# Kernel optimization log

Hardware: AMD Instinct MI355X
Metric: run time of the kernel (lower is better)

## Reference

```python
import jax, jax.numpy as jnp
import numpy as np

D_MODEL, D_STATE, D_CONV, EXPAND = 1024, 16, 4, 2
D_INNER = EXPAND * D_MODEL
B, L = 2, 2048


def setup_inputs() -> dict:
    key = jax.random.key(0)
    ks = jax.random.split(key, 8)
    s = lambda fan: 1.0 / np.sqrt(fan)
    x = jax.random.normal(ks[0], (B, L, D_MODEL), dtype=jnp.float32)
    W_in = jax.random.normal(ks[1], (2 * D_INNER, D_MODEL), dtype=jnp.float32) * s(D_MODEL)
    conv_w = jax.random.normal(ks[2], (D_INNER, 1, D_CONV), dtype=jnp.float32) * s(D_CONV)
    conv_b = jax.random.normal(ks[3], (D_INNER,), dtype=jnp.float32) * 0.01
    A_log = jnp.log(jnp.abs(jax.random.normal(ks[4], (D_INNER, D_STATE), dtype=jnp.float32)) + 1e-4)
    Dp = jnp.ones((D_INNER,), dtype=jnp.float32)
    W_dt = jax.random.normal(ks[5], (D_INNER, D_INNER), dtype=jnp.float32) * s(D_INNER)
    b_dt = jax.random.normal(ks[6], (D_INNER,), dtype=jnp.float32) * 0.01
    W_out = jax.random.normal(ks[7], (D_MODEL, D_INNER), dtype=jnp.float32) * s(D_INNER)
    return {"x": x, "W_in": W_in, "conv_w": conv_w, "conv_b": conv_b,
            "A_log": A_log, "Dp": Dp, "W_dt": W_dt, "b_dt": b_dt, "W_out": W_out}


def _mamba_fwd(x, W_in, conv_w, conv_b, A_log, Dp, W_dt, b_dt, W_out):
    Bsz, Ln, _ = x.shape
    xz = x @ W_in.T                                  # [B, L, 2*d_inner]
    x_proj, z = jnp.split(xz, 2, axis=-1)            # each [B, L, d_inner]
    # depthwise causal conv1d: left-pad d_conv-1 (matches torch pad + [:L] slice)
    xc = jnp.transpose(x_proj, (0, 2, 1))            # [B, C, L]
    xc = jax.lax.conv_general_dilated(
        xc, conv_w, window_strides=(1,), padding=[(D_CONV - 1, 0)],
        dimension_numbers=("NCH", "OIH", "NCH"), feature_group_count=D_INNER)
    xc = xc + conv_b[None, :, None]
    x_act = jax.nn.silu(jnp.transpose(xc, (0, 2, 1)))  # [B, L, d_inner]
    dt = jax.nn.softplus(x_act @ W_dt.T + b_dt)        # [B, L, d_inner]
    A = -jnp.exp(A_log)                                # [d_inner, d_state]

    def step(h, inp):
        xt, dt_t = inp                                 # [B, d_inner] each
        dA = jnp.exp(dt_t[:, :, None] * A[None])       # [B, d_inner, d_state]
        dB = (dt_t * xt)[:, :, None]                   # broadcast over states
        h = dA * h + dB
        y_t = h.sum(axis=-1) + Dp * xt                 # [B, d_inner]
        return h, y_t

    h0 = jnp.zeros((Bsz, D_INNER, D_STATE), dtype=x.dtype)
    xs = (jnp.transpose(x_act, (1, 0, 2)), jnp.transpose(dt, (1, 0, 2)))  # [L, B, d_inner]
    _, ys = jax.lax.scan(step, h0, xs)
    y_ssm = jnp.transpose(ys, (1, 0, 2))               # [B, L, d_inner]
    y_gated = y_ssm * jax.nn.silu(z)
    return y_gated @ W_out.T                           # [B, L, d_model]


def reference(x, W_in, conv_w, conv_b, A_log, Dp, W_dt, b_dt, W_out):
    return _mamba_fwd(x, W_in, conv_w, conv_b, A_log, Dp, W_dt, b_dt, W_out)
```

## Files before the change

### kernel.cpp

```cpp
#include <hip/hip_runtime.h>

#define DMODEL 1024
#define DSTATE 16
#define DCONV  4
#define DINNER 2048
#define BSZ    2
#define LSEQ   2048
#define MTOT   (BSZ * LSEQ)
#define NCH    64
#define LC     (LSEQ / NCH)
#define LOG2E  1.44269504088896f

typedef unsigned short u16;
typedef __attribute__((ext_vector_type(8))) short short8;
typedef __attribute__((ext_vector_type(8))) unsigned short u16x8;
typedef __attribute__((ext_vector_type(4))) float f32x4;

__device__ __forceinline__ float silu_f(float v) {
  return v * __builtin_amdgcn_rcpf(1.f + __builtin_amdgcn_exp2f(-v * LOG2E));
}

__device__ __forceinline__ u16 f2bf(float f) {
  unsigned int u = __float_as_uint(f);
  u += 0x7FFF + ((u >> 16) & 1);
  return (u16)(u >> 16);
}
__device__ __forceinline__ float bf2f(u16 b) { return __uint_as_float(((unsigned int)b) << 16); }

__device__ __forceinline__ void gload_lds16(const u16* g, u16* l) {
  __builtin_amdgcn_global_load_lds((const __attribute__((address_space(1))) unsigned int*)g,
                                   (__attribute__((address_space(3))) unsigned int*)l, 16, 0, 0);
}

__global__ __launch_bounds__(256)
void cast4(const float4* __restrict__ s0, ushort4* __restrict__ d0, int n0,
           const float4* __restrict__ s1, ushort4* __restrict__ d1, int n1,
           const float4* __restrict__ s2, ushort4* __restrict__ d2, int n2,
           const float4* __restrict__ s3, ushort4* __restrict__ d3, int n3) {
  int i = blockIdx.x * 256 + threadIdx.x;
  const float4* s; ushort4* d;
  if (i < n0)                { s = s0; d = d0; }
  else if ((i -= n0) < n1)   { s = s1; d = d1; }
  else if ((i -= n1) < n2)   { s = s2; d = d2; }
  else if ((i -= n2) < n3)   { s = s3; d = d3; }
  else return;
  float4 v = s[i];
  ushort4 o = { f2bf(v.x), f2bf(v.y), f2bf(v.z), f2bf(v.w) };
  d[i] = o;
}

template<int OBF>
__global__ __launch_bounds__(256, 2)
void hgemm256(const u16* __restrict__ A, const u16* __restrict__ B,
              void* __restrict__ Cv, int M, int N, int K) {
  __shared__ u16 As[256 * 64];
  __shared__ u16 Bs[128 * 64];
  const int tid  = threadIdx.x;
  const int lane = tid & 63;
  const int w    = tid >> 6;
  const int quad = lane >> 4;
  const int l16  = lane & 15;

  const int nbn = N >> 7, nbm = M >> 8;
  const int pid = blockIdx.x;
  const int npg = 4 * nbn;
  const int fm  = (pid / npg) * 4;
  const int gsz = (nbm - fm < 4) ? (nbm - fm) : 4;
  const int bm  = (fm + (pid % gsz)) << 8;
  const int bn  = ((pid % npg) / gsz) << 7;

  const int wm = (w & 1) * 128;
  const int wn = (w >> 1) * 64;

  const int rseg = lane >> 3;
  const int cd   = (lane & 7) ^ rseg;
  const u16* Gp[12]; u16* Lp[12];
#pragma unroll
  for (int q = 0; q < 12; ++q) {
    const int g = w * 12 + q;
    if (g < 32) {
      const int r = g * 8 + rseg;
      Gp[q] = A + (size_t)(bm + r) * K + (cd << 3);
      Lp[q] = &As[g << 9];
    } else {
      const int r = (g - 32) * 8 + rseg;
      Gp[q] = B + (size_t)(bn + r) * K + (cd << 3);
      Lp[q] = &Bs[(g - 32) << 9];
    }
  }

  const short8* Afp[8][2];
  const short8* Bfp[4][2];
#pragma unroll
  for (int t = 0; t < 8; ++t) {
    const int ra = wm + 16 * t + l16;
#pragma unroll
    for (int ks = 0; ks < 2; ++ks)
      Afp[t][ks] = (const short8*)&As[ra * 64 + (((quad + 4 * ks) ^ (ra & 7)) << 3)];
  }
#pragma unroll
  for (int t = 0; t < 4; ++t) {
    const int rb = wn + 16 * t + l16;
#pragma unroll
    for (int ks = 0; ks < 2; ++ks)
      Bfp[t][ks] = (const short8*)&Bs[rb * 64 + (((quad + 4 * ks) ^ (rb & 7)) << 3)];
  }

  f32x4 acc[8][4] = {};

  for (int k0 = 0; k0 < K; k0 += 64) {
#pragma unroll
    for (int q = 0; q < 12; ++q) { gload_lds16(Gp[q], Lp[q]); Gp[q] += 64; }
    __syncthreads();
#pragma unroll
    for (int ks = 0; ks < 2; ++ks) {
      short8 af[8], bf[4];
#pragma unroll
      for (int t = 0; t < 8; ++t) af[t] = *Afp[t][ks];
#pragma unroll
      for (int t = 0; t < 4; ++t) bf[t] = *Bfp[t][ks];
#pragma unroll
      for (int ti = 0; ti < 8; ++ti)
#pragma unroll
        for (int tj = 0; tj < 4; ++tj)
          acc[ti][tj] = __builtin_amdgcn_mfma_f32_16x16x32_bf16(af[ti], bf[tj],
                                                                acc[ti][tj], 0, 0, 0);
    }
    __syncthreads();
  }

#pragma unroll
  for (int ti = 0; ti < 8; ++ti) {
    const int row0 = bm + wm + 16 * ti + quad * 4;
#pragma unroll
    for (int tj = 0; tj < 4; ++tj) {
      const int col = bn + wn + 16 * tj + l16;
#pragma unroll
      for (int i = 0; i < 4; ++i) {
        const float v = acc[ti][tj][i];
        if (OBF) ((u16*)Cv)[(size_t)(row0 + i) * N + col] = f2bf(v);
        else     ((float*)Cv)[(size_t)(row0 + i) * N + col] = v;
      }
    }
  }
}

template<int MODE, int OBF, int BN>
__global__ __launch_bounds__(256)
void hgemm_bk128(const u16* __restrict__ A, const u16* __restrict__ B,
                 const float* __restrict__ bias, void* __restrict__ Cv,
                 int M, int N, int K) {
  constexpr int ASEG = 32;
  constexpr int BSEG = BN / 4;
  constexpr int SPW  = (ASEG + BSEG) / 4;
  constexpr int BT   = BN / 32;
  __shared__ u16 As[128 * 128];
  __shared__ u16 Bs[BN * 128];
  const int tid  = threadIdx.x;
  const int lane = tid & 63;
  const int w    = tid >> 6;
  const int quad = lane >> 4;
  const int l16  = lane & 15;

  const int nbn = N / BN, nbm = M >> 7;
  const int pid = blockIdx.x;
  const int npg = 4 * nbn;
  const int fm  = (pid / npg) * 4;
  const int gsz = (nbm - fm < 4) ? (nbm - fm) : 4;
  const int bm  = (fm + (pid % gsz)) << 7;
  const int bn  = ((pid % npg) / gsz) * BN;

  const int wm = (w & 1) * 64;
  const int wn = (w >> 1) * (BN / 2);

  const int rs4 = lane >> 4;
  const u16* Gp[SPW]; u16* Lp[SPW];
#pragma unroll
  for (int q = 0; q < SPW; ++q) {
    const int g = w * SPW + q;
    if (g < ASEG) {
      const int r  = g * 4 + rs4;
      const int cdk = (lane & 15) ^ (r & 15);
      Gp[q] = A + (size_t)(bm + r) * K + (cdk << 3);
      Lp[q] = &As[g << 9];
    } else {
      const int r  = (g - ASEG) * 4 + rs4;
      const int cdk = (lane & 15) ^ (r & 15);
      Gp[q] = B + (size_t)(bn + r) * K + (cdk << 3);
      Lp[q] = &Bs[(g - ASEG) << 9];
    }
  }

  const short8* Afp[4][4];
  const short8* Bfp[BT][4];
#pragma unroll
  for (int t = 0; t < 4; ++t) {
    const int ra = wm + 16 * t + l16;
#pragma unroll
    for (int ks = 0; ks < 4; ++ks)
      Afp[t][ks] = (const short8*)&As[ra * 128 + (((quad + 4 * ks) ^ (ra & 15)) << 3)];
  }
#pragma unroll
  for (int t = 0; t < BT; ++t) {
    const int rb = wn + 16 * t + l16;
#pragma unroll
    for (int ks = 0; ks < 4; ++ks)
      Bfp[t][ks] = (const short8*)&Bs[rb * 128 + (((quad + 4 * ks) ^ (rb & 15)) << 3)];
  }

  f32x4 acc[4][BT] = {};

  for (int k0 = 0; k0 < K; k0 += 128) {
#pragma unroll
    for (int q = 0; q < SPW; ++q) { gload_lds16(Gp[q], Lp[q]); Gp[q] += 128; }
    __syncthreads();
#pragma unroll
    for (int ks = 0; ks < 4; ++ks) {
      short8 af[4], bf[BT];
#pragma unroll
      for (int t = 0; t < 4; ++t) af[t] = *Afp[t][ks];
#pragma unroll
      for (int t = 0; t < BT; ++t) bf[t] = *Bfp[t][ks];
#pragma unroll
      for (int ti = 0; ti < 4; ++ti)
#pragma unroll
        for (int tj = 0; tj < BT; ++tj)
          acc[ti][tj] = __builtin_amdgcn_mfma_f32_16x16x32_bf16(af[ti], bf[tj],
                                                                acc[ti][tj], 0, 0, 0);
    }
    __syncthreads();
  }

#pragma unroll
  for (int ti = 0; ti < 4; ++ti) {
    const int row0 = bm + wm + 16 * ti + quad * 4;
#pragma unroll
    for (int tj = 0; tj < BT; ++tj) {
      const int col = bn + wn + 16 * tj + l16;
      const float bv = (MODE == 1) ? bias[col] : 0.f;
#pragma unroll
      for (int i = 0; i < 4; ++i) {
        float v = acc[ti][tj][i] + bv;
        if (MODE == 1) v = (v > 20.f) ? v : __logf(1.f + __expf(v));
        if (OBF) ((u16*)Cv)[(size_t)(row0 + i) * N + col] = f2bf(v);
        else     ((float*)Cv)[(size_t)(row0 + i) * N + col] = v;
      }
    }
  }
}

__global__ __launch_bounds__(256)
void conv_silu(const u16* __restrict__ xz, const float* __restrict__ conv_w,
               const float* __restrict__ conv_b, u16* __restrict__ xact) {
  const int i = blockIdx.x * 256 + threadIdx.x;
  const int ko = i & 255;
  const int t  = (i >> 8) & (LSEQ - 1);
  const int b  = i >> 19;
  const int c  = ko << 3;
  float a[8];
  float4 w[8];
#pragma unroll
  for (int j = 0; j < 8; ++j) {
    a[j] = conv_b[c + j];
    w[j] = *(const float4*)(conv_w + (c + j) * DCONV);
  }
#pragma unroll
  for (int k = 0; k < DCONV; ++k) {
    const int tt = t + k - (DCONV - 1);
    if (tt >= 0) {
      const u16x8 v = *(const u16x8*)(xz + ((size_t)(b * LSEQ + tt) << 12) + c);
#pragma unroll
      for (int j = 0; j < 8; ++j)
        a[j] = fmaf(bf2f(v[j]), ((const float*)&w[j])[k], a[j]);
    }
  }
  u16x8 o;
#pragma unroll
  for (int j = 0; j < 8; ++j) o[j] = f2bf(silu_f(a[j]));
  *(u16x8*)(xact + ((size_t)(b * LSEQ + t) << 11) + c) = o;
}


__global__ __launch_bounds__(256, 2)
void scan_pass1(const u16* __restrict__ dtb, const u16* __restrict__ xact,
                const float* __restrict__ A_log,
                u16* __restrict__ hbuf, float* __restrict__ sumdt) {
  const int gid = blockIdx.x * 256 + threadIdx.x;
  const int c  = gid & (DINNER - 1);
  const int ch = (gid >> 11) & (NCH - 1);
  const int b  = gid >> 17;
  float a2[16];
#pragma unroll
  for (int s = 0; s < 16; ++s)
    a2[s] = -__expf(A_log[c * DSTATE + s]) * LOG2E;
  const size_t base = ((size_t)(b * LSEQ + ch * LC) << 11) + c;
  float h[16] = {};
  float sd = 0.f;
  for (int j = 0; j < LC; j += 2) {
    const float dt0 = bf2f(dtb [base + ((size_t)j << 11)]);
    const float xv0 = bf2f(xact[base + ((size_t)j << 11)]);
    const float dt1 = bf2f(dtb [base + ((size_t)(j + 1) << 11)]);
    const float xv1 = bf2f(xact[base + ((size_t)(j + 1) << 11)]);
    const float dx0 = dt0 * xv0, dx1 = dt1 * xv1;
    sd += dt0 + dt1;
#pragma unroll
    for (int s = 0; s < 16; ++s)
      h[s] = fmaf(__builtin_amdgcn_exp2f(dt0 * a2[s]), h[s], dx0);
#pragma unroll
    for (int s = 0; s < 16; ++s)
      h[s] = fmaf(__builtin_amdgcn_exp2f(dt1 * a2[s]), h[s], dx1);
  }
  u16x8* ho = (u16x8*)&hbuf[(((size_t)(b * NCH + ch) * DINNER) + c) << 4];
  u16x8 lo, hi;
#pragma unroll
  for (int s = 0; s < 8; ++s) { lo[s] = f2bf(h[s]); hi[s] = f2bf(h[8 + s]); }
  ho[0] = lo; ho[1] = hi;
  sumdt[(size_t)(b * NCH + ch) * DINNER + c] = sd;
}

__global__ __launch_bounds__(256)
void scan_combine(u16* __restrict__ hbuf, const float* __restrict__ sumdt,
                  const float* __restrict__ A_log) {
  const int gid = blockIdx.x * 256 + threadIdx.x;
  const int s = gid & 15;
  const int c = (gid >> 4) & (DINNER - 1);
  const int b = gid >> 15;
  const float a2 = -__expf(A_log[c * DSTATE + s]) * LOG2E;
  float h = 0.f;
  for (int k = 0; k < NCH; ++k) {
    const size_t o = (((size_t)(b * NCH + k) * DINNER) + c) * 16 + s;
    const float he = bf2f(hbuf[o]);
    const float sd = sumdt[(size_t)(b * NCH + k) * DINNER + c];
    hbuf[o] = f2bf(h);
    h = fmaf(__builtin_amdgcn_exp2f(sd * a2), h, he);
  }
}

__global__ __launch_bounds__(256, 2)
void scan_pass3(const u16* __restrict__ dtb, const u16* __restrict__ xact,
                const u16* __restrict__ xz, const float* __restrict__ A_log,
                const float* __restrict__ Dp, const u16* __restrict__ hbuf,
                u16* __restrict__ yg) {
  const int gid = blockIdx.x * 256 + threadIdx.x;
  const int c  = gid & (DINNER - 1);
  const int ch = (gid >> 11) & (NCH - 1);
  const int b  = gid >> 17;
  float a2[16];
#pragma unroll
  for (int s = 0; s < 16; ++s)
    a2[s] = -__expf(A_log[c * DSTATE + s]) * LOG2E;
  const float dp = Dp[c];
  float h[16];
  const u16x8* hi = (const u16x8*)&hbuf[(((size_t)(b * NCH + ch) * DINNER) + c) << 4];
  const u16x8 vlo = hi[0], vhi = hi[1];
#pragma unroll
  for (int s = 0; s < 8; ++s) { h[s] = bf2f(vlo[s]); h[8 + s] = bf2f(vhi[s]); }
  const size_t base  = ((size_t)(b * LSEQ + ch * LC) << 11) + c;
  const size_t zbase = ((size_t)(b * LSEQ + ch * LC) << 12) + DINNER + c;
  for (int j = 0; j < LC; j += 2) {
    const float dt0 = bf2f(dtb [base + ((size_t)j << 11)]);
    const float xv0 = bf2f(xact[base + ((size_t)j << 11)]);
    const float zv0 = bf2f(xz[zbase + ((size_t)j << 12)]);
    const float dt1 = bf2f(dtb [base + ((size_t)(j + 1) << 11)]);
    const float xv1 = bf2f(xact[base + ((size_t)(j + 1) << 11)]);
    const float zv1 = bf2f(xz[zbase + ((size_t)(j + 1) << 12)]);
    const float dx0 = dt0 * xv0, dx1 = dt1 * xv1;
    float y0 = 0.f, y1 = 0.f;
#pragma unroll
    for (int s = 0; s < 16; ++s) {
      h[s] = fmaf(__builtin_amdgcn_exp2f(dt0 * a2[s]), h[s], dx0);
      y0 += h[s];
    }
#pragma unroll
    for (int s = 0; s < 16; ++s) {
      h[s] = fmaf(__builtin_amdgcn_exp2f(dt1 * a2[s]), h[s], dx1);
      y1 += h[s];
    }
    y0 = fmaf(dp, xv0, y0);
    y1 = fmaf(dp, xv1, y1);
    yg[base + ((size_t)j << 11)]       = f2bf(y0 * silu_f(zv0));
    yg[base + ((size_t)(j + 1) << 11)] = f2bf(y1 * silu_f(zv1));
  }
}

extern "C" void kernel_launch(void* const* d_in, const int* in_sizes, int n_in,
                              void* d_out, int out_size, void* d_ws, size_t ws_size,
                              hipStream_t stream) {
  const float* x      = (const float*)d_in[0];
  const float* W_in   = (const float*)d_in[1];
  const float* conv_w = (const float*)d_in[2];
  const float* conv_b = (const float*)d_in[3];
  const float* A_log  = (const float*)d_in[4];
  const float* Dp     = (const float*)d_in[5];
  const float* W_dt   = (const float*)d_in[6];
  const float* b_dt   = (const float*)d_in[7];
  const float* W_out  = (const float*)d_in[8];
  float* out = (float*)d_out;

  u16* xz   = (u16*)d_ws;
  u16* dtb  = xz   + (size_t)MTOT * 2 * DINNER;
  u16* xbf  = dtb  + (size_t)MTOT * DINNER;
  u16* wibf = xbf  + (size_t)MTOT * DMODEL;
  u16* wdbf = wibf + (size_t)2 * DINNER * DMODEL;
  u16* wobf = wdbf + (size_t)DINNER * DINNER;
  u16* xact = wobf + (size_t)DMODEL * DINNER;
  u16* yg   = xact + (size_t)MTOT * DINNER;
  u16* hbuf = yg   + (size_t)MTOT * DINNER;
  float* sumdt = (float*)(hbuf + (size_t)BSZ * NCH * DINNER * 16);

  const dim3 blk(256);

  const int n0 = MTOT * DMODEL / 4, n1 = 2 * DINNER * DMODEL / 4;
  const int n2 = DINNER * DINNER / 4, n3 = DMODEL * DINNER / 4;
  cast4<<<(n0 + n1 + n2 + n3) / 256, blk, 0, stream>>>(
      (const float4*)x, (ushort4*)xbf, n0,
      (const float4*)W_in, (ushort4*)wibf, n1,
      (const float4*)W_dt, (ushort4*)wdbf, n2,
      (const float4*)W_out, (ushort4*)wobf, n3);

  hgemm256<1><<<(MTOT / 256) * (2 * DINNER / 128), blk, 0, stream>>>(
      xbf, wibf, xz, MTOT, 2 * DINNER, DMODEL);
  conv_silu<<<(MTOT * 256) / 256, blk, 0, stream>>>(xz, conv_w, conv_b, xact);
  hgemm_bk128<1, 1, 128><<<(MTOT / 128) * (DINNER / 128), blk, 0, stream>>>(
      xact, wdbf, b_dt, dtb, MTOT, DINNER, DINNER);
  scan_pass1<<<BSZ * NCH * DINNER / 256, blk, 0, stream>>>(dtb, xact, A_log, hbuf, sumdt);
  scan_combine<<<BSZ * DINNER * 16 / 256, blk, 0, stream>>>(hbuf, sumdt, A_log);
  scan_pass3<<<BSZ * NCH * DINNER / 256, blk, 0, stream>>>(dtb, xact, xz, A_log, Dp, hbuf, yg);
  hgemm_bk128<0, 0, 64><<<(MTOT / 128) * (DMODEL / 64), blk, 0, stream>>>(
      yg, wobf, nullptr, out, MTOT, DMODEL, DINNER);
}
```

Before: 306.2 us.

## Replace input and dt GEMMs with 8-wave double-buffered pipelined GEMM kernel

Result: no change. 309.8 us (+1.2%).

```diff
diff --git a/kernel.cpp b/kernel.cpp
--- a/kernel.cpp
+++ b/kernel.cpp
@@ -49,97 +49,133 @@
   d[i] = o;
 }
 
-template<int OBF>
-__global__ __launch_bounds__(256, 2)
-void hgemm256(const u16* __restrict__ A, const u16* __restrict__ B,
-              void* __restrict__ Cv, int M, int N, int K) {
-  __shared__ u16 As[256 * 64];
-  __shared__ u16 Bs[128 * 64];
+template<int BN, int MODE, int OBF>
+__global__ __launch_bounds__(512, 2)
+void gemm8p(const u16* __restrict__ A, const u16* __restrict__ Bm,
+            const float* __restrict__ bias, void* __restrict__ Cv,
+            int M, int N, int K) {
+  constexpr int BT  = BN / 32;
+  constexpr int TJP = BT / 4;
+  constexpr int NBH = BN / 128;
+  extern __shared__ __align__(16) u16 smem[];
+  u16* As = smem;
+  u16* Bs = smem + 2 * 256 * 64;
+
   const int tid  = threadIdx.x;
   const int lane = tid & 63;
   const int w    = tid >> 6;
   const int quad = lane >> 4;
   const int l16  = lane & 15;
-
-  const int nbn = N >> 7, nbm = M >> 8;
+  const int wm   = (w >> 1) * 64;
+  const int wn   = (w & 1) * (BN / 2);
+
+  const int nbn = N / BN;
   const int pid = blockIdx.x;
-  const int npg = 4 * nbn;
-  const int fm  = (pid / npg) * 4;
-  const int gsz = (nbm - fm < 4) ? (nbm - fm) : 4;
-  const int bm  = (fm + (pid % gsz)) << 8;
-  const int bn  = ((pid % npg) / gsz) << 7;
-
-  const int wm = (w & 1) * 128;
-  const int wn = (w >> 1) * 64;
+  const int bm  = (pid / nbn) << 8;
+  const int bn  = (pid % nbn) * BN;
 
   const int rseg = lane >> 3;
-  const int cd   = (lane & 7) ^ rseg;
-  const u16* Gp[12]; u16* Lp[12];
-#pragma unroll
-  for (int q = 0; q < 12; ++q) {
-    const int g = w * 12 + q;
-    if (g < 32) {
-      const int r = g * 8 + rseg;
-      Gp[q] = A + (size_t)(bm + r) * K + (cd << 3);
-      Lp[q] = &As[g << 9];
-    } else {
-      const int r = (g - 32) * 8 + rseg;
-      Gp[q] = B + (size_t)(bn + r) * K + (cd << 3);
-      Lp[q] = &Bs[(g - 32) << 9];
-    }
-  }
-
-  const short8* Afp[8][2];
-  const short8* Bfp[4][2];
-#pragma unroll
-  for (int t = 0; t < 8; ++t) {
+  const int cd8  = (((lane & 7) ^ rseg) << 3);
+  const u16* gA = A  + (size_t)(bm + 16 * w + rseg) * K + cd8;
+  const u16* gB = Bm + (size_t)(bn + 16 * w + rseg) * K + cd8;
+  u16* lA = &As[(2 * w) << 9];
+  u16* lB = &Bs[(2 * w) << 9];
+  const int Kmask = K - 1;
+
+  auto stA = [&](int slot, int h, int kt) {
+    const size_t go = (size_t)h * 128 * K + ((kt << 6) & Kmask);
+    gload_lds16(gA + go,         lA + slot * 16384 + h * 8192);
+    gload_lds16(gA + go + 8 * K, lA + slot * 16384 + h * 8192 + 512);
+  };
+  auto stB = [&](int slot, int h, int kt) {
+    const size_t go = (size_t)h * 128 * K + ((kt << 6) & Kmask);
+    gload_lds16(gB + go,         lB + slot * (BN * 64) + h * 8192);
+    gload_lds16(gB + go + 8 * K, lB + slot * (BN * 64) + h * 8192 + 512);
+  };
+
+  int aoff[4][2], boff[BT][2];
+#pragma unroll
+  for (int t = 0; t < 4; ++t) {
     const int ra = wm + 16 * t + l16;
 #pragma unroll
     for (int ks = 0; ks < 2; ++ks)
-      Afp[t][ks] = (const short8*)&As[ra * 64 + (((quad + 4 * ks) ^ (ra & 7)) << 3)];
-  }
+      aoff[t][ks] = ra * 64 + (((quad + 4 * ks) ^ (ra & 7)) << 3);
+  }
+#pragma unroll
+  for (int tj = 0; tj < BT; ++tj) {
+    const int rb = wn + 16 * tj + l16;
+#pragma unroll
+    for (int ks = 0; ks < 2; ++ks)
+      boff[tj][ks] = rb * 64 + (((quad + 4 * ks) ^ (rb & 7)) << 3);
+  }
+
+  f32x4 acc[4][BT] = {};
+  short8 af[4][2];
+
+#define RD_AF(slot)                                                          \
+  { _Pragma("unroll") for (int t = 0; t < 4; ++t)                            \
+      _Pragma("unroll") for (int ks = 0; ks < 2; ++ks)                       \
+        af[t][ks] = *(const short8*)&As[(slot) * 16384 + aoff[t][ks]]; }
+
+#define PHASE(slot, j, STG)                                                  \
+  {                                                                          \
+    if ((j) == 0) RD_AF(slot);                                               \
+    short8 bfp[TJP][2];                                                      \
+    _Pragma("unroll") for (int jj = 0; jj < TJP; ++jj)                       \
+      _Pragma("unroll") for (int ks = 0; ks < 2; ++ks)                       \
+        bfp[jj][ks] = *(const short8*)&Bs[(slot) * (BN * 64) +               \
+                                          boff[(j) * TJP + jj][ks]];         \
+    STG;                                                                     \
+    __builtin_amdgcn_s_barrier();                                            \
+    __builtin_amdgcn_s_setprio(1);                                           \
+    _Pragma("unroll") for (int ks = 0; ks < 2; ++ks)                         \
+      _Pragma("unroll") for (int jj = 0; jj < TJP; ++jj)                     \
+        _Pragma("unroll") for (int t = 0; t < 4; ++t)                        \
+          acc[t][(j) * TJP + jj] = __builtin_amdgcn_mfma_f32_16x16x32_bf16(  \
+              af[t][ks], bfp[jj][ks], acc[t][(j) * TJP + jj], 0, 0, 0);      \
+    __builtin_amdgcn_s_setprio(0);                                           \
+    asm volatile("s_waitcnt lgkmcnt(0)" ::: "memory");                       \
+    __builtin_amdgcn_s_barrier();                                            \
+  }
+
+  stA(0, 0, 0); stA(0, 1, 0);
+  stB(0, 0, 0); if (NBH == 2) stB(0, 1, 0);
+  stA(1, 0, 1); stA(1, 1, 1);
+  asm volatile("s_waitcnt vmcnt(4)" ::: "memory");
+  __builtin_amdgcn_s_barrier();
+
+  const int niter = K >> 7;
+  for (int i = 0; i < niter; ++i) {
+    const int tb1 = 2 * i + 1, t2 = 2 * i + 2, t3 = 2 * i + 3;
+    PHASE(0, 0, { stB(1, 0, tb1); });
+    PHASE(0, 1, { if (NBH == 2) stB(1, 1, tb1); stA(0, 0, t2); });
+    PHASE(0, 2, { stA(0, 1, t2); });
+    PHASE(0, 3, {});
+    asm volatile("s_waitcnt vmcnt(4)" ::: "memory");
+    PHASE(1, 0, { stB(0, 0, t2); });
+    PHASE(1, 1, { if (NBH == 2) stB(0, 1, t2); stA(1, 0, t3); });
+    PHASE(1, 2, { stA(1, 1, t3); });
+    PHASE(1, 3, {});
+    asm volatile("s_waitcnt vmcnt(4)" ::: "memory");
+  }
+#undef PHASE
+#undef RD_AF
+
+  asm volatile("s_waitcnt vmcnt(0)" ::: "memory");
+
 #pragma unroll
   for (int t = 0; t < 4; ++t) {
-    const int rb = wn + 16 * t + l16;
-#pragma unroll
-    for (int ks = 0; ks < 2; ++ks)
-      Bfp[t][ks] = (const short8*)&Bs[rb * 64 + (((quad + 4 * ks) ^ (rb & 7)) << 3)];
-  }
-
-  f32x4 acc[8][4] = {};
-
-  for (int k0 = 0; k0 < K; k0 += 64) {
-#pragma unroll
-    for (int q = 0; q < 12; ++q) { gload_lds16(Gp[q], Lp[q]); Gp[q] += 64; }
-    __syncthreads();
-#pragma unroll
-    for (int ks = 0; ks < 2; ++ks) {
-      short8 af[8], bf[4];
-#pragma unroll
-      for (int t = 0; t < 8; ++t) af[t] = *Afp[t][ks];
-#pragma unroll
-      for (int t = 0; t < 4; ++t) bf[t] = *Bfp[t][ks];
-#pragma unroll
-      for (int ti = 0; ti < 8; ++ti)
-#pragma unroll
-        for (int tj = 0; tj < 4; ++tj)
-          acc[ti][tj] = __builtin_amdgcn_mfma_f32_16x16x32_bf16(af[ti], bf[tj],
-                                                                acc[ti][tj], 0, 0, 0);
-    }
-    __syncthreads();
-  }
-
-#pragma unroll
-  for (int ti = 0; ti < 8; ++ti) {
-    const int row0 = bm + wm + 16 * ti + quad * 4;
-#pragma unroll
-    for (int tj = 0; tj < 4; ++tj) {
+    const int row0 = bm + wm + 16 * t + quad * 4;
+#pragma unroll
+    for (int tj = 0; tj < BT; ++tj) {
       const int col = bn + wn + 16 * tj + l16;
-#pragma unroll
-      for (int i = 0; i < 4; ++i) {
-        const float v = acc[ti][tj][i];
-        if (OBF) ((u16*)Cv)[(size_t)(row0 + i) * N + col] = f2bf(v);
-        else     ((float*)Cv)[(size_t)(row0 + i) * N + col] = v;
+      const float bv = (MODE == 1) ? bias[col] : 0.f;
+#pragma unroll
+      for (int i2 = 0; i2 < 4; ++i2) {
+        float v = acc[t][tj][i2] + bv;
+        if (MODE == 1) v = (v > 20.f) ? v : __logf(1.f + __expf(v));
+        if (OBF) ((u16*)Cv)[(size_t)(row0 + i2) * N + col] = f2bf(v);
+        else     ((float*)Cv)[(size_t)(row0 + i2) * N + col] = v;
       }
     }
   }
@@ -410,6 +446,15 @@
 
   const dim3 blk(256);
 
+  static bool s_attr = false;
+  if (!s_attr) {
+    hipFuncSetAttribute(reinterpret_cast<const void*>(&gemm8p<256, 0, 1>),
+                        hipFuncAttributeMaxDynamicSharedMemorySize, 131072);
+    hipFuncSetAttribute(reinterpret_cast<const void*>(&gemm8p<128, 1, 1>),
+                        hipFuncAttributeMaxDynamicSharedMemorySize, 98304);
+    s_attr = true;
+  }
+
   const int n0 = MTOT * DMODEL / 4, n1 = 2 * DINNER * DMODEL / 4;
   const int n2 = DINNER * DINNER / 4, n3 = DMODEL * DINNER / 4;
   cast4<<<(n0 + n1 + n2 + n3) / 256, blk, 0, stream>>>(
@@ -418,10 +463,10 @@
       (const float4*)W_dt, (ushort4*)wdbf, n2,
       (const float4*)W_out, (ushort4*)wobf, n3);
 
-  hgemm256<1><<<(MTOT / 256) * (2 * DINNER / 128), blk, 0, stream>>>(
-      xbf, wibf, xz, MTOT, 2 * DINNER, DMODEL);
+  gemm8p<256, 0, 1><<<(MTOT / 256) * (2 * DINNER / 256), dim3(512), 131072, stream>>>(
+      xbf, wibf, nullptr, xz, MTOT, 2 * DINNER, DMODEL);
   conv_silu<<<(MTOT * 256) / 256, blk, 0, stream>>>(xz, conv_w, conv_b, xact);
-  hgemm_bk128<1, 1, 128><<<(MTOT / 128) * (DINNER / 128), blk, 0, stream>>>(
+  gemm8p<128, 1, 1><<<(MTOT / 256) * (DINNER / 128), dim3(512), 98304, stream>>>(
       xact, wdbf, b_dt, dtb, MTOT, DINNER, DINNER);
   scan_pass1<<<BSZ * NCH * DINNER / 256, blk, 0, stream>>>(dtb, xact, A_log, hbuf, sumdt);
   scan_combine<<<BSZ * DINNER * 16 / 256, blk, 0, stream>>>(hbuf, sumdt, A_log);
```
